# Optimization experiments

Measured on AMD Instinct MI355X. Metric: run time of the kernel, lower is better.

The kernel has to match this reference:

```python
import jax, jax.numpy as jnp
import numpy as np

N = 50000      # nodes
E = 800000     # edges
R = 8          # relation types
IN = 128       # in_dim
OUT = 128      # out_dim
H = 8          # num_heads
HD = OUT // H  # head dim = 16


def setup_inputs() -> dict:
    key = jax.random.key(0)
    ks = jax.random.split(key, 6)
    return {
        "h": jax.random.normal(ks[0], (N, IN), dtype=jnp.float32),
        "fc_weight": jax.random.normal(ks[1], (R, IN, OUT), dtype=jnp.float32) * 0.05,
        "attn_weight": jax.random.normal(ks[2], (R, H, 2 * HD), dtype=jnp.float32) * 0.05,
        "src": jax.random.randint(ks[3], (E,), 0, N, dtype=jnp.int32),
        "dst": jax.random.randint(ks[4], (E,), 0, N, dtype=jnp.int32),
        "etype": jax.random.randint(ks[5], (E,), 0, R, dtype=jnp.int32),
    }


def reference(h, fc_weight, attn_weight, src, dst, etype):
    # Per-relation projection of ALL node features (equivalent math to the
    # per-edge gathered bmm in the original, without materializing E x IN x OUT):
    # [R, N, OUT] -> [R, N, H, HD]
    z_nodes = jnp.einsum('ni,rio->rno', h, fc_weight).reshape(R, N, H, HD)
    z_s = z_nodes[etype, src]   # [E, H, HD]  (== bmm(h[src], fc_weight[etype]))
    z_d = z_nodes[etype, dst]   # [E, H, HD]
    aw = attn_weight[etype]     # [E, H, 2*HD]
    # a = sum(cat([z_s, z_d], -1) * attn_weight[etype], -1)
    a = jnp.sum(z_s * aw[:, :, :HD], axis=2) + jnp.sum(z_d * aw[:, :, HD:], axis=2)  # [E, H]
    e = jax.nn.leaky_relu(a)    # torch F.leaky_relu_ default slope 0.01

    # Edge softmax per destination node (per head), numerically stable.
    m = jax.ops.segment_max(e, dst, num_segments=N)          # [N, H]
    m = jnp.where(jnp.isfinite(m), m, jnp.zeros_like(m))     # guard empty nodes
    ex = jnp.exp(e - m[dst])                                 # [E, H]
    denom = jax.ops.segment_sum(ex, dst, num_segments=N)     # [N, H]
    num = jax.ops.segment_sum(ex[:, :, None] * z_s, dst, num_segments=N)  # [N, H, HD]
    out = num / jnp.maximum(denom, 1e-9)[:, :, None]         # [N, H, HD]
    return out
```

## Files before the change

kernel.cpp:

```cpp
#include <hip/hip_runtime.h>

#define NN 50000
#define NE 800000
#define NR 8
#define DIN 128
#define DOUT 128
#define NH 8

#define NB_SCAN ((NN + 255) / 256)

typedef __attribute__((ext_vector_type(8))) short bf16x8;
typedef __attribute__((ext_vector_type(4))) float f32x4;

__device__ __forceinline__ unsigned short f2bf(float f) {
  unsigned u = __float_as_uint(f);
  unsigned r = (u + 0x7FFFu + ((u >> 16) & 1u)) >> 16;
  return (unsigned short)r;
}
__device__ __forceinline__ float bf2f(unsigned short b) {
  return __uint_as_float(((unsigned)b) << 16);
}

__global__ __launch_bounds__(256) void prep_hb(const float* __restrict__ h,
                                               unsigned short* __restrict__ hb) {
  int i = blockIdx.x * 256 + threadIdx.x;
  if (i >= NN * DIN / 8) return;
  const float4* p = (const float4*)(h + (size_t)i * 8);
  float4 v0 = p[0], v1 = p[1];
  ushort4 w0, w1;
  w0.x = f2bf(v0.x); w0.y = f2bf(v0.y); w0.z = f2bf(v0.z); w0.w = f2bf(v0.w);
  w1.x = f2bf(v1.x); w1.y = f2bf(v1.y); w1.z = f2bf(v1.z); w1.w = f2bf(v1.w);
  ushort4* o = (ushort4*)(hb + (size_t)i * 8);
  o[0] = w0; o[1] = w1;
}

__global__ __launch_bounds__(256) void prep_fcf(
    const float* __restrict__ fc, const float* __restrict__ attn,
    unsigned short* __restrict__ fcf) {
  int idx = blockIdx.x * 256 + threadIdx.x;
  if (idx >= NR * DIN * 144) return;
  int r = idx / (DIN * 144);
  int rem = idx - r * (DIN * 144);
  int k = rem / 144;
  int j = rem - k * 144;
  float v;
  if (j < DOUT) {
    v = fc[((size_t)r * DIN + k) * DOUT + j];
  } else {
    int cc = j - DOUT;
    int hh = cc & 7, p = cc >> 3;
    const float* fr = fc + ((size_t)r * DIN + k) * DOUT + hh * 16;
    const float* ar = attn + ((size_t)r * NH + hh) * 32 + p * 16;
    v = 0.f;
#pragma unroll
    for (int d = 0; d < 16; ++d) v += fr[d] * ar[d];
  }
  int t = j >> 4, c = j & 15, ks = k >> 5, gg = (k >> 3) & 3, i = k & 7;
  fcf[((((size_t)r * 9 + t) * 4 + ks) * 4 + gg) * 128 + c * 8 + i] = f2bf(v);
}

__global__ __launch_bounds__(256) void gemm_mfma(
    const unsigned short* __restrict__ hb, const unsigned short* __restrict__ fcf,
    unsigned short* __restrict__ z, float* __restrict__ s_buf) {
  const int r = blockIdx.y;
  const int n0 = blockIdx.x * 64;
  const int w = threadIdx.x >> 6;
  const int lane = threadIdx.x & 63;
  const int g = lane >> 4, c = lane & 15;
  const int nbase = n0 + w * 16;

  bf16x8 bf[9][4];
  const unsigned short* fb = fcf + ((size_t)r * 36 * 64 + lane) * 8;
#pragma unroll
  for (int t = 0; t < 9; ++t)
#pragma unroll
    for (int ks = 0; ks < 4; ++ks)
      bf[t][ks] = *(const bf16x8*)(fb + (size_t)(t * 4 + ks) * 512);

  int arow = nbase + c;
  if (arow > NN - 1) arow = NN - 1;
  const unsigned short* ha = hb + (size_t)arow * DIN + g * 8;
  bf16x8 af[4];
#pragma unroll
  for (int ks = 0; ks < 4; ++ks) af[ks] = *(const bf16x8*)(ha + ks * 32);

  f32x4 acc[9];
#pragma unroll
  for (int t = 0; t < 9; ++t) acc[t] = (f32x4){0.f, 0.f, 0.f, 0.f};

#pragma unroll
  for (int ks = 0; ks < 4; ++ks)
#pragma unroll
    for (int t = 0; t < 9; ++t)
      acc[t] = __builtin_amdgcn_mfma_f32_16x16x32_bf16(bf[t][ks], af[ks], acc[t], 0, 0, 0);

  int node = nbase + c;
  if (node < NN) {
    unsigned short* zr = z + ((size_t)r * NN + node) * DOUT + g * 4;
#pragma unroll
    for (int t = 0; t < 8; ++t) {
      ushort4 wv;
      wv.x = f2bf(acc[t][0]); wv.y = f2bf(acc[t][1]);
      wv.z = f2bf(acc[t][2]); wv.w = f2bf(acc[t][3]);
      *(ushort4*)(zr + t * 16) = wv;
    }
    float* sb = s_buf + ((size_t)r * NN + node) * 16 + g * 4;
    *(float4*)sb = make_float4(acc[8][0], acc[8][1], acc[8][2], acc[8][3]);
  }
}

__global__ __launch_bounds__(256) void hist_kernel(const int* __restrict__ dst,
                                                   int* __restrict__ deg) {
  int e = blockIdx.x * blockDim.x + threadIdx.x;
  if (e < NE) atomicAdd(&deg[dst[e]], 1);
}

__global__ __launch_bounds__(256) void scan1(const int* __restrict__ deg,
                                             int* __restrict__ bsum) {
  __shared__ int ws_[4];
  int gi = blockIdx.x * 256 + threadIdx.x;
  int v = (gi < NN) ? deg[gi] : 0;
#pragma unroll
  for (int m = 1; m < 64; m <<= 1) v += __shfl_xor(v, m);
  if ((threadIdx.x & 63) == 0) ws_[threadIdx.x >> 6] = v;
  __syncthreads();
  if (threadIdx.x == 0) bsum[blockIdx.x] = ws_[0] + ws_[1] + ws_[2] + ws_[3];
}

__global__ __launch_bounds__(256) void scan2(const int* __restrict__ bsum,
                                             int* __restrict__ bbase,
                                             int* __restrict__ row_start) {
  __shared__ int part[256];
  int t = threadIdx.x;
  part[t] = (t < NB_SCAN) ? bsum[t] : 0;
  __syncthreads();
  for (int off = 1; off < 256; off <<= 1) {
    int v = (t >= off) ? part[t - off] : 0;
    __syncthreads();
    part[t] += v;
    __syncthreads();
  }
  if (t < NB_SCAN) bbase[t] = (t == 0) ? 0 : part[t - 1];
  if (t == 0) row_start[NN] = NE;
}

__global__ __launch_bounds__(256) void scan3(const int* __restrict__ deg,
                                             const int* __restrict__ bbase,
                                             int* __restrict__ row_start) {
  __shared__ int part[256];
  int t = threadIdx.x;
  int gi = blockIdx.x * 256 + t;
  int v = (gi < NN) ? deg[gi] : 0;
  part[t] = v;
  __syncthreads();
  for (int off = 1; off < 256; off <<= 1) {
    int x = (t >= off) ? part[t - off] : 0;
    __syncthreads();
    part[t] += x;
    __syncthreads();
  }
  if (gi < NN) row_start[gi] = bbase[blockIdx.x] + part[t] - v;
}

__global__ __launch_bounds__(256) void scatter_kernel(
    const int* __restrict__ src, const int* __restrict__ dst,
    const int* __restrict__ et, const float* __restrict__ s_buf,
    const int* __restrict__ row_start, int* __restrict__ cursor,
    unsigned short* __restrict__ es, unsigned* __restrict__ sidx) {
  int e = blockIdx.x * blockDim.x + threadIdx.x;
  if (e >= NE) return;
  int s = src[e], d = dst[e], r = et[e];
  int pos = row_start[d] + atomicAdd(&cursor[d], 1);
  const float4* sp = (const float4*)&s_buf[((size_t)r * NN + s) * 16];
  const float4* dp = (const float4*)&s_buf[((size_t)r * NN + d) * 16 + 8];
  float4 a0 = sp[0], a1 = sp[1], b0 = dp[0], b1 = dp[1];
  float ev[8] = {a0.x + b0.x, a0.y + b0.y, a0.z + b0.z, a0.w + b0.w,
                 a1.x + b1.x, a1.y + b1.y, a1.z + b1.z, a1.w + b1.w};
  ushort4 w0, w1;
  unsigned short wv[8];
#pragma unroll
  for (int hh = 0; hh < 8; ++hh) {
    float x = ev[hh];
    x = x > 0.f ? x : 0.01f * x;
    wv[hh] = f2bf(x);
  }
  w0.x = wv[0]; w0.y = wv[1]; w0.z = wv[2]; w0.w = wv[3];
  w1.x = wv[4]; w1.y = wv[5]; w1.z = wv[6]; w1.w = wv[7];
  *(ushort4*)&es[(size_t)pos * 8] = w0;
  *(ushort4*)&es[(size_t)pos * 8 + 4] = w1;
  sidx[pos] = (unsigned)s | ((unsigned)r << 16);
}

__global__ __launch_bounds__(256) void node_accum(
    const int* __restrict__ row_start, const unsigned short* __restrict__ es,
    const unsigned* __restrict__ sidx, const unsigned short* __restrict__ z,
    float* __restrict__ out) {
  int wave = threadIdx.x >> 6;
  int lane = threadIdx.x & 63;
  int n = blockIdx.x * 4 + wave;
  if (n >= NN) return;
  int b0 = row_start[n];
  int deg = row_start[n + 1] - b0;

  int hl = lane & 7;
  int jg = lane >> 3;
  int c16 = lane & 15;
  int e4 = lane >> 4;

  float maxv = -INFINITY;
  for (int j = jg; j < deg; j += 8)
    maxv = fmaxf(maxv, bf2f(es[(size_t)(b0 + j) * 8 + hl]));
#pragma unroll
  for (int m = 8; m < 64; m <<= 1) maxv = fmaxf(maxv, __shfl_xor(maxv, m));

  float acc[8] = {0.f, 0.f, 0.f, 0.f, 0.f, 0.f, 0.f, 0.f};
  float den = 0.f;
  int hh16 = c16 >> 1;

  for (int cch = 0; cch < deg; cch += 8) {
    int j = cch + jg;
    float ex = 0.f;
    if (j < deg) ex = __expf(bf2f(es[(size_t)(b0 + j) * 8 + hl]) - maxv);
    den += ex;
    int rem = min(8, deg - cch);
    unsigned pk = sidx[b0 + cch + min(lane & 7, rem - 1)];
#pragma unroll
    for (int half = 0; half < 2; ++half) {
      if (half * 4 >= rem) break;
      int o = half * 4 + e4;
      float exb = __shfl(ex, (o << 3) | hh16);
      unsigned p = __shfl(pk, o);
      unsigned sr_ = p & 0xFFFFu;
      unsigned rr = p >> 16;
      bf16x8 v = *(const bf16x8*)&z[(((size_t)rr * NN + sr_) << 7) + c16 * 8];
#pragma unroll
      for (int i = 0; i < 8; ++i)
        acc[i] += exb * bf2f((unsigned short)v[i]);
    }
  }
#pragma unroll
  for (int m = 8; m < 64; m <<= 1) den += __shfl_xor(den, m);
#pragma unroll
  for (int i = 0; i < 8; ++i) {
    acc[i] += __shfl_xor(acc[i], 16);
    acc[i] += __shfl_xor(acc[i], 32);
  }
  float deno = __shfl(den, hh16);
  float inv = 1.0f / fmaxf(deno, 1e-9f);
  if (lane < 16) {
    float* ob = out + ((size_t)n << 7) + lane * 8;
    *(float4*)ob = make_float4(acc[0] * inv, acc[1] * inv, acc[2] * inv, acc[3] * inv);
    *(float4*)(ob + 4) = make_float4(acc[4] * inv, acc[5] * inv, acc[6] * inv, acc[7] * inv);
  }
}

extern "C" void kernel_launch(void* const* d_in, const int* in_sizes, int n_in,
                              void* d_out, int out_size, void* d_ws, size_t ws_size,
                              hipStream_t stream) {
  const float* h = (const float*)d_in[0];
  const float* fc = (const float*)d_in[1];
  const float* attn = (const float*)d_in[2];
  const int* src = (const int*)d_in[3];
  const int* dst = (const int*)d_in[4];
  const int* et = (const int*)d_in[5];
  float* out = (float*)d_out;

  char* wsb = (char*)d_ws;
  size_t off = 0;
  unsigned short* z = (unsigned short*)(wsb + off);  off += (size_t)NR * NN * DOUT * 2;
  unsigned short* hb = (unsigned short*)(wsb + off); off += (size_t)NN * DIN * 2;
  float* s_buf = (float*)(wsb + off);                off += (size_t)NR * NN * 16 * 4;
  unsigned short* es = (unsigned short*)(wsb + off); off += (size_t)NE * NH * 2;
  unsigned* sidx = (unsigned*)(wsb + off);           off += (size_t)NE * 4;
  unsigned short* fcf = (unsigned short*)(wsb + off);off += (size_t)NR * 9 * 4 * 4 * 128 * 2;
  int* deg = (int*)(wsb + off);                      off += (size_t)NN * 4;
  int* row_start = (int*)(wsb + off);                off += (size_t)(NN + 1) * 4;
  int* cursor = (int*)(wsb + off);                   off += (size_t)NN * 4;
  int* bsum = (int*)(wsb + off);                     off += (size_t)NB_SCAN * 4;
  int* bbase = (int*)(wsb + off);                    off += (size_t)NB_SCAN * 4;

  hipMemsetAsync(deg, 0, (size_t)NN * sizeof(int), stream);
  hipMemsetAsync(cursor, 0, (size_t)NN * sizeof(int), stream);

  prep_hb<<<(NN * DIN / 8 + 255) / 256, 256, 0, stream>>>(h, hb);
  prep_fcf<<<(NR * DIN * 144 + 255) / 256, 256, 0, stream>>>(fc, attn, fcf);

  dim3 ggrid((NN + 63) / 64, NR);
  gemm_mfma<<<ggrid, 256, 0, stream>>>(hb, fcf, z, s_buf);

  hist_kernel<<<(NE + 255) / 256, 256, 0, stream>>>(dst, deg);
  scan1<<<NB_SCAN, 256, 0, stream>>>(deg, bsum);
  scan2<<<1, 256, 0, stream>>>(bsum, bbase, row_start);
  scan3<<<NB_SCAN, 256, 0, stream>>>(deg, bbase, row_start);

  scatter_kernel<<<(NE + 255) / 256, 256, 0, stream>>>(src, dst, et, s_buf,
                                                       row_start, cursor, es, sidx);

  node_accum<<<(NN + 3) / 4, 256, 0, stream>>>(row_start, es, sidx, z, out);
}
```

Measured before the change: 311.8 us.

## Fuse bf16 conversion of h into GEMM, loop relations in-block, store scores as bf16

Removes the prep_hb kernel: the GEMM now reads fp32 h directly and converts it to bf16 in registers. Each block loops over all 8 relations, so the A fragment is loaded once per node tile instead of once per relation, and B fragments are streamed from global/L2 per MFMA rather than preloaded. The attention score buffer is stored as bf16 instead of fp32, halving its write and gather traffic in scatter_kernel. The trade-offs are lower precision on the attention logits and fewer blocks (no relation grid dimension), with B loads now sitting in the MFMA loop.

```diff
diff --git a/kernel.cpp b/kernel.cpp
--- a/kernel.cpp
+++ b/kernel.cpp
@@ -19,19 +19,6 @@
 }
 __device__ __forceinline__ float bf2f(unsigned short b) {
   return __uint_as_float(((unsigned)b) << 16);
-}
-
-__global__ __launch_bounds__(256) void prep_hb(const float* __restrict__ h,
-                                               unsigned short* __restrict__ hb) {
-  int i = blockIdx.x * 256 + threadIdx.x;
-  if (i >= NN * DIN / 8) return;
-  const float4* p = (const float4*)(h + (size_t)i * 8);
-  float4 v0 = p[0], v1 = p[1];
-  ushort4 w0, w1;
-  w0.x = f2bf(v0.x); w0.y = f2bf(v0.y); w0.z = f2bf(v0.z); w0.w = f2bf(v0.w);
-  w1.x = f2bf(v1.x); w1.y = f2bf(v1.y); w1.z = f2bf(v1.z); w1.w = f2bf(v1.w);
-  ushort4* o = (ushort4*)(hb + (size_t)i * 8);
-  o[0] = w0; o[1] = w1;
 }
 
 __global__ __launch_bounds__(256) void prep_fcf(
@@ -60,52 +47,60 @@
 }
 
 __global__ __launch_bounds__(256) void gemm_mfma(
-    const unsigned short* __restrict__ hb, const unsigned short* __restrict__ fcf,
-    unsigned short* __restrict__ z, float* __restrict__ s_buf) {
-  const int r = blockIdx.y;
+    const float* __restrict__ h, const unsigned short* __restrict__ fcf,
+    unsigned short* __restrict__ z, unsigned short* __restrict__ s_buf) {
   const int n0 = blockIdx.x * 64;
   const int w = threadIdx.x >> 6;
   const int lane = threadIdx.x & 63;
   const int g = lane >> 4, c = lane & 15;
   const int nbase = n0 + w * 16;
 
-  bf16x8 bf[9][4];
-  const unsigned short* fb = fcf + ((size_t)r * 36 * 64 + lane) * 8;
-#pragma unroll
-  for (int t = 0; t < 9; ++t)
-#pragma unroll
-    for (int ks = 0; ks < 4; ++ks)
-      bf[t][ks] = *(const bf16x8*)(fb + (size_t)(t * 4 + ks) * 512);
-
   int arow = nbase + c;
   if (arow > NN - 1) arow = NN - 1;
-  const unsigned short* ha = hb + (size_t)arow * DIN + g * 8;
+  const float* ha = h + (size_t)arow * DIN + g * 8;
   bf16x8 af[4];
 #pragma unroll
-  for (int ks = 0; ks < 4; ++ks) af[ks] = *(const bf16x8*)(ha + ks * 32);
-
-  f32x4 acc[9];
-#pragma unroll
-  for (int t = 0; t < 9; ++t) acc[t] = (f32x4){0.f, 0.f, 0.f, 0.f};
-
-#pragma unroll
-  for (int ks = 0; ks < 4; ++ks)
-#pragma unroll
-    for (int t = 0; t < 9; ++t)
-      acc[t] = __builtin_amdgcn_mfma_f32_16x16x32_bf16(bf[t][ks], af[ks], acc[t], 0, 0, 0);
-
-  int node = nbase + c;
-  if (node < NN) {
-    unsigned short* zr = z + ((size_t)r * NN + node) * DOUT + g * 4;
-#pragma unroll
-    for (int t = 0; t < 8; ++t) {
-      ushort4 wv;
-      wv.x = f2bf(acc[t][0]); wv.y = f2bf(acc[t][1]);
-      wv.z = f2bf(acc[t][2]); wv.w = f2bf(acc[t][3]);
-      *(ushort4*)(zr + t * 16) = wv;
+  for (int ks = 0; ks < 4; ++ks) {
+    float4 v0 = *(const float4*)(ha + ks * 32);
+    float4 v1 = *(const float4*)(ha + ks * 32 + 4);
+    bf16x8 a;
+    a[0] = (short)f2bf(v0.x); a[1] = (short)f2bf(v0.y);
+    a[2] = (short)f2bf(v0.z); a[3] = (short)f2bf(v0.w);
+    a[4] = (short)f2bf(v1.x); a[5] = (short)f2bf(v1.y);
+    a[6] = (short)f2bf(v1.z); a[7] = (short)f2bf(v1.w);
+    af[ks] = a;
+  }
+
+  const int node = nbase + c;
+
+  for (int r = 0; r < NR; ++r) {
+    const unsigned short* fb = fcf + ((size_t)r * 36 * 64 + lane) * 8;
+    f32x4 acc[9];
+#pragma unroll
+    for (int t = 0; t < 9; ++t) acc[t] = (f32x4){0.f, 0.f, 0.f, 0.f};
+
+#pragma unroll
+    for (int ks = 0; ks < 4; ++ks)
+#pragma unroll
+      for (int t = 0; t < 9; ++t) {
+        bf16x8 bf = *(const bf16x8*)(fb + (size_t)(t * 4 + ks) * 512);
+        acc[t] = __builtin_amdgcn_mfma_f32_16x16x32_bf16(bf, af[ks], acc[t], 0, 0, 0);
+      }
+
+    if (node < NN) {
+      unsigned short* zr = z + ((size_t)r * NN + node) * DOUT + g * 4;
+#pragma unroll
+      for (int t = 0; t < 8; ++t) {
+        ushort4 wv;
+        wv.x = f2bf(acc[t][0]); wv.y = f2bf(acc[t][1]);
+        wv.z = f2bf(acc[t][2]); wv.w = f2bf(acc[t][3]);
+        *(ushort4*)(zr + t * 16) = wv;
+      }
+      ushort4 sv;
+      sv.x = f2bf(acc[8][0]); sv.y = f2bf(acc[8][1]);
+      sv.z = f2bf(acc[8][2]); sv.w = f2bf(acc[8][3]);
+      *(ushort4*)&s_buf[((size_t)r * NN + node) * 16 + g * 4] = sv;
     }
-    float* sb = s_buf + ((size_t)r * NN + node) * 16 + g * 4;
-    *(float4*)sb = make_float4(acc[8][0], acc[8][1], acc[8][2], acc[8][3]);
   }
 }
 
@@ -164,18 +159,21 @@
 
 __global__ __launch_bounds__(256) void scatter_kernel(
     const int* __restrict__ src, const int* __restrict__ dst,
-    const int* __restrict__ et, const float* __restrict__ s_buf,
+    const int* __restrict__ et, const unsigned short* __restrict__ s_buf,
     const int* __restrict__ row_start, int* __restrict__ cursor,
     unsigned short* __restrict__ es, unsigned* __restrict__ sidx) {
   int e = blockIdx.x * blockDim.x + threadIdx.x;
   if (e >= NE) return;
   int s = src[e], d = dst[e], r = et[e];
   int pos = row_start[d] + atomicAdd(&cursor[d], 1);
-  const float4* sp = (const float4*)&s_buf[((size_t)r * NN + s) * 16];
-  const float4* dp = (const float4*)&s_buf[((size_t)r * NN + d) * 16 + 8];
-  float4 a0 = sp[0], a1 = sp[1], b0 = dp[0], b1 = dp[1];
-  float ev[8] = {a0.x + b0.x, a0.y + b0.y, a0.z + b0.z, a0.w + b0.w,
-                 a1.x + b1.x, a1.y + b1.y, a1.z + b1.z, a1.w + b1.w};
+  ushort4 sa0 = *(const ushort4*)&s_buf[((size_t)r * NN + s) * 16];
+  ushort4 sa1 = *(const ushort4*)&s_buf[((size_t)r * NN + s) * 16 + 4];
+  ushort4 sb0 = *(const ushort4*)&s_buf[((size_t)r * NN + d) * 16 + 8];
+  ushort4 sb1 = *(const ushort4*)&s_buf[((size_t)r * NN + d) * 16 + 12];
+  float ev[8] = {bf2f(sa0.x) + bf2f(sb0.x), bf2f(sa0.y) + bf2f(sb0.y),
+                 bf2f(sa0.z) + bf2f(sb0.z), bf2f(sa0.w) + bf2f(sb0.w),
+                 bf2f(sa1.x) + bf2f(sb1.x), bf2f(sa1.y) + bf2f(sb1.y),
+                 bf2f(sa1.z) + bf2f(sb1.z), bf2f(sa1.w) + bf2f(sb1.w)};
   ushort4 w0, w1;
   unsigned short wv[8];
 #pragma unroll
@@ -267,26 +265,23 @@
 
   char* wsb = (char*)d_ws;
   size_t off = 0;
-  unsigned short* z = (unsigned short*)(wsb + off);  off += (size_t)NR * NN * DOUT * 2;
-  unsigned short* hb = (unsigned short*)(wsb + off); off += (size_t)NN * DIN * 2;
-  float* s_buf = (float*)(wsb + off);                off += (size_t)NR * NN * 16 * 4;
-  unsigned short* es = (unsigned short*)(wsb + off); off += (size_t)NE * NH * 2;
-  unsigned* sidx = (unsigned*)(wsb + off);           off += (size_t)NE * 4;
-  unsigned short* fcf = (unsigned short*)(wsb + off);off += (size_t)NR * 9 * 4 * 4 * 128 * 2;
-  int* deg = (int*)(wsb + off);                      off += (size_t)NN * 4;
-  int* row_start = (int*)(wsb + off);                off += (size_t)(NN + 1) * 4;
-  int* cursor = (int*)(wsb + off);                   off += (size_t)NN * 4;
-  int* bsum = (int*)(wsb + off);                     off += (size_t)NB_SCAN * 4;
-  int* bbase = (int*)(wsb + off);                    off += (size_t)NB_SCAN * 4;
+  unsigned short* z = (unsigned short*)(wsb + off);    off += (size_t)NR * NN * DOUT * 2;
+  unsigned short* s_buf = (unsigned short*)(wsb + off);off += (size_t)NR * NN * 16 * 2;
+  unsigned short* es = (unsigned short*)(wsb + off);   off += (size_t)NE * NH * 2;
+  unsigned* sidx = (unsigned*)(wsb + off);             off += (size_t)NE * 4;
+  unsigned short* fcf = (unsigned short*)(wsb + off);  off += (size_t)NR * 9 * 4 * 4 * 128 * 2;
+  int* deg = (int*)(wsb + off);                        off += (size_t)NN * 4;
+  int* row_start = (int*)(wsb + off);                  off += (size_t)(NN + 1) * 4;
+  int* cursor = (int*)(wsb + off);                     off += (size_t)NN * 4;
+  int* bsum = (int*)(wsb + off);                       off += (size_t)NB_SCAN * 4;
+  int* bbase = (int*)(wsb + off);                      off += (size_t)NB_SCAN * 4;
 
   hipMemsetAsync(deg, 0, (size_t)NN * sizeof(int), stream);
   hipMemsetAsync(cursor, 0, (size_t)NN * sizeof(int), stream);
 
-  prep_hb<<<(NN * DIN / 8 + 255) / 256, 256, 0, stream>>>(h, hb);
   prep_fcf<<<(NR * DIN * 144 + 255) / 256, 256, 0, stream>>>(fc, attn, fcf);
 
-  dim3 ggrid((NN + 63) / 64, NR);
-  gemm_mfma<<<ggrid, 256, 0, stream>>>(hb, fcf, z, s_buf);
+  gemm_mfma<<<(NN + 63) / 64, 256, 0, stream>>>(h, fcf, z, s_buf);
 
   hist_kernel<<<(NE + 255) / 256, 256, 0, stream>>>(dst, deg);
   scan1<<<NB_SCAN, 256, 0, stream>>>(deg, bsum);
```

New measurement: 308.1 us. About the same (-1.2%).
